# Performance work log

Measured on AMD Instinct MI355X. Metric: run time of the kernel, lower is better.

Reference implementation:

```python
import jax, jax.numpy as jnp
import numpy as np

VOCAB, X, H, C_CLS = 32000, 300, 512, 5
B, N_LEAVES = 256, 256  # complete binary trees, depth 9, 511 nodes/tree

def setup_inputs() -> dict:
    key = jax.random.key(0)
    ks = jax.random.split(key, 10)
    s = lambda k, shp, fan: jax.random.normal(k, shp, jnp.float32) * (1.0 / np.sqrt(fan))
    return {
        'wordid': jax.random.randint(ks[0], (B, N_LEAVES), 0, VOCAB),
        'emb': jax.random.normal(ks[1], (VOCAB, X), jnp.float32) * 0.1,
        'W_iou_w': s(ks[2], (3 * H, X), X),
        'W_iou_b': jnp.zeros((3 * H,), jnp.float32),
        'U_iou_w': s(ks[3], (3 * H, 2 * H), 2 * H),
        'U_iou_b': jnp.zeros((3 * H,), jnp.float32),
        'U_f_w': s(ks[4], (2 * H, 2 * H), 2 * H),
        'U_f_b': jnp.zeros((2 * H,), jnp.float32),
        'lin_w': s(ks[5], (C_CLS, H), H),
        'lin_b': jnp.zeros((C_CLS,), jnp.float32),
    }

def _cell(iou, c_f):
    i, o, u = jnp.split(iou, 3, axis=-1)
    c = jax.nn.sigmoid(i) * jnp.tanh(u) + c_f
    h = jax.nn.sigmoid(o) * jnp.tanh(c)
    return h, c

def reference(wordid, emb, W_iou_w, W_iou_b, U_iou_w, U_iou_b, U_f_w, U_f_b, lin_w, lin_b):
    b, n = wordid.shape
    # leaves: is_leaf=1 -> iou = W_iou(x), c_f = 0
    x = emb[wordid]                                   # [B, L, X]
    iou = x @ W_iou_w.T + W_iou_b                     # [B, L, 3H]
    h, c = _cell(iou, 0.0)
    hs = [h]
    # internal levels: reduce over exactly 2 children (binary TreeLSTM)
    while h.shape[1] > 1:
        m = h.shape[1] // 2
        h_cat = h.reshape(b, m, 2 * H)                # concat of 2 children
        c_pair = c.reshape(b, m, 2, H)
        f = jax.nn.sigmoid(h_cat @ U_f_w.T + U_f_b).reshape(b, m, 2, H)
        c_f = jnp.sum(f * c_pair, axis=2)             # [B, m, H]
        iou = h_cat @ U_iou_w.T + U_iou_b             # is_leaf=0 branch
        h, c = _cell(iou, c_f)
        hs.append(h)
    h_all = jnp.concatenate(hs, axis=1)               # [B, 2L-1, H], leaves-first topo order
    # dropout is identity at inference
    logits = h_all @ lin_w.T + lin_b                  # [B, 2L-1, num_classes]
    return logits
```

## Files before the change

kernel.cpp:

```cpp
#include <hip/hip_runtime.h>
#include <hip/hip_bf16.h>


typedef __bf16 bf16;
typedef bf16  bf16x8 __attribute__((ext_vector_type(8)));
typedef float f32x4  __attribute__((ext_vector_type(4)));

__device__ __forceinline__ float sigm(float x){ return 1.0f/(1.0f + __expf(-x)); }
__device__ __forceinline__ float tanh_f(float x){ return 1.0f - 2.0f/(__expf(2.0f*x)+1.0f); }

__device__ __forceinline__ void gload16(const bf16* g, bf16* l){
  __builtin_amdgcn_global_load_lds(
      (const __attribute__((address_space(1))) void*)g,
      (__attribute__((address_space(3))) void*)l, 16, 0, 0);
}

#define FENCE_LGKM do{ asm volatile("s_waitcnt lgkmcnt(0)" ::: "memory"); \
  __builtin_amdgcn_sched_barrier(0); __builtin_amdgcn_s_barrier(); \
  __builtin_amdgcn_sched_barrier(0); }while(0)
#define FENCE_VM(N) do{ asm volatile("s_waitcnt vmcnt(" #N ")" ::: "memory"); \
  __builtin_amdgcn_sched_barrier(0); __builtin_amdgcn_s_barrier(); \
  __builtin_amdgcn_sched_barrier(0); }while(0)

__global__ void cvt_all(const float* __restrict__ Wiou, const float* __restrict__ Uiou,
                        const float* __restrict__ Uf, const float* __restrict__ emb,
                        bf16* __restrict__ Wpad, bf16* __restrict__ Uall,
                        bf16* __restrict__ embp){
  const int b = blockIdx.x, t = threadIdx.x;
  if (b < 1536){
    Wpad[b*320 + t] = (bf16)(t < 300 ? Wiou[b*300 + t] : 0.f);
  } else if (b < 1536 + 32000){
    const int r = b - 1536;
    embp[(size_t)r*320 + t] = (bf16)(t < 300 ? emb[(size_t)r*300 + t] : 0.f);
  } else {
    const size_t i = (size_t)(b - 33536)*320 + t;
    if (i < (size_t)1536*1024) Uall[i] = (bf16)Uiou[i];
    else                       Uall[i] = (bf16)Uf[i - (size_t)1536*1024];
  }
}

__global__ __launch_bounds__(256, 2)
void leaf128_kernel(const int* __restrict__ wordid, const bf16* __restrict__ embp,
                    const bf16* __restrict__ Wpad, const float* __restrict__ Wb,
                    bf16* __restrict__ hcur, float* __restrict__ ccur)
{
  __shared__ bf16 lsA[2][128*32];
  __shared__ bf16 lsB[2][192*32];
  const int t = threadIdx.x;
  const int mrow0 = blockIdx.x*128, nblk = blockIdx.y*64;
  const int lane16 = t&15, quad = (t&63)>>4, w = t>>6;

  const int lrow = t>>2;
  const int qsw  = ((t&3) ^ ((t>>3)&3))*8;
  const int wb   = (t & 192)*8;

  const int wid0 = wordid[mrow0 + lrow];
  const int wid1 = wordid[mrow0 + 64 + lrow];
  const bf16* srcA0 = embp + (size_t)wid0*320 + qsw;
  const bf16* srcA1 = embp + (size_t)wid1*320 + qsw;
  const bf16* srcB0 = Wpad + (size_t)(0*512 + nblk + lrow)*320 + qsw;
  const bf16* srcB1 = Wpad + (size_t)(1*512 + nblk + lrow)*320 + qsw;
  const bf16* srcB2 = Wpad + (size_t)(2*512 + nblk + lrow)*320 + qsw;

  const int sA   = (t>>1)&3;
  const int aoff = lane16*32 + ((quad ^ sA)*8);
  const int boff = (w*16 + lane16)*32 + ((quad ^ sA)*8);

  f32x4 acc[3][8];
  const f32x4 zero = {0.f,0.f,0.f,0.f};
  #pragma unroll
  for(int o=0;o<3;o++){
    #pragma unroll
    for(int rt=0;rt<8;rt++) acc[o][rt]=zero;
  }

  {
    gload16(srcA0     , lsA[0] + wb);        gload16(srcA1     , lsA[0] + 2048 + wb);
    gload16(srcB0     , lsB[0] + wb);        gload16(srcB1     , lsB[0] + 2048 + wb);
    gload16(srcB2     , lsB[0] + 4096 + wb);
    gload16(srcA0 + 32, lsA[1] + wb);        gload16(srcA1 + 32, lsA[1] + 2048 + wb);
    gload16(srcB0 + 32, lsB[1] + wb);        gload16(srcB1 + 32, lsB[1] + 2048 + wb);
    gload16(srcB2 + 32, lsB[1] + 4096 + wb);
  }
  FENCE_VM(5);

  for (int ks = 0; ks < 10; ks++){
    const int cur = ks & 1;
    bf16x8 bfrag[3], afrag[8];
    #pragma unroll
    for(int g=0;g<3;g++) bfrag[g] = *(const bf16x8*)&lsB[cur][g*2048 + boff];
    #pragma unroll
    for(int rt=0;rt<8;rt++) afrag[rt] = *(const bf16x8*)&lsA[cur][rt*512 + aoff];
    FENCE_LGKM;
    if (ks < 8){
      const int k0 = (ks+2)*32;
      gload16(srcA0 + k0, lsA[cur] + wb);        gload16(srcA1 + k0, lsA[cur] + 2048 + wb);
      gload16(srcB0 + k0, lsB[cur] + wb);        gload16(srcB1 + k0, lsB[cur] + 2048 + wb);
      gload16(srcB2 + k0, lsB[cur] + 4096 + wb);
    }
    __builtin_amdgcn_s_setprio(1);
    #pragma unroll
    for(int rt=0;rt<8;rt++){
      #pragma unroll
      for(int g=0;g<3;g++)
        acc[g][rt] = __builtin_amdgcn_mfma_f32_16x16x32_bf16(afrag[rt], bfrag[g], acc[g][rt], 0,0,0);
    }
    __builtin_amdgcn_s_setprio(0);
    if (ks < 8)      FENCE_VM(5);
    else if (ks < 9) FENCE_VM(0);
  }
  const int j = nblk + w*16 + lane16;
  const float bi=Wb[j], bo=Wb[512+j], bu=Wb[1024+j];
  #pragma unroll
  for(int rt=0;rt<8;rt++){
    #pragma unroll
    for(int reg=0;reg<4;reg++){
      const int row = mrow0 + rt*16 + quad*4 + reg;
      float iv=acc[0][rt][reg]+bi, ov=acc[1][rt][reg]+bo, uv=acc[2][rt][reg]+bu;
      float c = sigm(iv)*tanh_f(uv);
      float h = sigm(ov)*tanh_f(c);
      ccur[(size_t)row*512 + j] = c;
      hcur[(size_t)row*512 + j] = (bf16)h;
    }
  }
}

__global__ __launch_bounds__(256)
void level_kernel(const bf16* __restrict__ hprev, bf16* __restrict__ hcur,
                  const float* __restrict__ cprev, float* __restrict__ ccur,
                  const bf16* __restrict__ Uall, const float* __restrict__ Uioub,
                  const float* __restrict__ Ufb)
{
  __shared__ bf16 lsA[64*40];
  __shared__ bf16 lsB[5][64*40];
  const int t = threadIdx.x;
  const int mrow0 = blockIdx.x*64, nblk = blockIdx.y*64;
  const int r = t>>2, kc = (t&3)*8;
  const int lane16 = t&15, quad = (t&63)>>4, w = t>>6;

  f32x4 acc[5][4];
  const f32x4 zero = {0.f,0.f,0.f,0.f};
  #pragma unroll
  for(int o=0;o<5;o++){
    #pragma unroll
    for(int rt=0;rt<4;rt++) acc[o][rt]=zero;
  }

  const bf16* arow = hprev + (size_t)(mrow0 + r)*1024;
  const int col = nblk + r;
  for (int k0=0;k0<1024;k0+=32){
    *(bf16x8*)&lsA[r*40+kc] = *(const bf16x8*)&arow[k0+kc];
    #pragma unroll
    for(int g=0;g<5;g++)
      *(bf16x8*)&lsB[g][r*40+kc] = *(const bf16x8*)&Uall[(size_t)(g*512+col)*1024 + k0+kc];
    __syncthreads();
    bf16x8 bfrag[5];
    #pragma unroll
    for(int o=0;o<5;o++) bfrag[o] = *(const bf16x8*)&lsB[o][(w*16+lane16)*40 + quad*8];
    #pragma unroll
    for(int rt=0;rt<4;rt++){
      bf16x8 a = *(const bf16x8*)&lsA[(rt*16+lane16)*40 + quad*8];
      #pragma unroll
      for(int o=0;o<5;o++)
        acc[o][rt] = __builtin_amdgcn_mfma_f32_16x16x32_bf16(a, bfrag[o], acc[o][rt], 0,0,0);
    }
    __syncthreads();
  }
  const int j = nblk + w*16 + lane16;
  const float bi =Uioub[j], bo=Uioub[512+j], bu=Uioub[1024+j];
  const float bfl=Ufb[j],   bfr=Ufb[512+j];
  #pragma unroll
  for(int rt=0;rt<4;rt++){
    #pragma unroll
    for(int reg=0;reg<4;reg++){
      const int row = mrow0 + rt*16 + quad*4 + reg;
      float iv=acc[0][rt][reg]+bi, ov=acc[1][rt][reg]+bo, uv=acc[2][rt][reg]+bu;
      float fl=acc[3][rt][reg]+bfl, fr=acc[4][rt][reg]+bfr;
      float cl = cprev[((size_t)row*2  )*512 + j];
      float cr = cprev[((size_t)row*2+1)*512 + j];
      float cf = sigm(fl)*cl + sigm(fr)*cr;
      float c  = sigm(iv)*tanh_f(uv) + cf;
      float h  = sigm(ov)*tanh_f(c);
      ccur[(size_t)row*512 + j] = c;
      hcur[(size_t)row*512 + j] = (bf16)h;
    }
  }
}

__global__ __launch_bounds__(256, 2)
void level128_kernel(const bf16* __restrict__ hprev, bf16* __restrict__ hcur,
                     const float* __restrict__ cprev, float* __restrict__ ccur,
                     const bf16* __restrict__ Uall, const float* __restrict__ Uioub,
                     const float* __restrict__ Ufb)
{
  __shared__ bf16 lsA[2][128*32];
  __shared__ bf16 lsB[2][320*32];
  const int t = threadIdx.x;
  const int mrow0 = blockIdx.x*128, nblk = blockIdx.y*64;
  const int lane16 = t&15, quad = (t&63)>>4, w = t>>6;

  const int lrow = t>>2;
  const int qsw  = ((t&3) ^ ((t>>3)&3))*8;
  const int wb   = (t & 192)*8;

  const bf16* srcA0 = hprev + (size_t)(mrow0 + lrow)*1024 + qsw;
  const bf16* srcA1 = hprev + (size_t)(mrow0 + 64 + lrow)*1024 + qsw;
  const bf16* srcB0 = Uall + (size_t)(0*512 + nblk + lrow)*1024 + qsw;
  const bf16* srcB1 = Uall + (size_t)(1*512 + nblk + lrow)*1024 + qsw;
  const bf16* srcB2 = Uall + (size_t)(2*512 + nblk + lrow)*1024 + qsw;
  const bf16* srcB3 = Uall + (size_t)(3*512 + nblk + lrow)*1024 + qsw;
  const bf16* srcB4 = Uall + (size_t)(4*512 + nblk + lrow)*1024 + qsw;

  const int sA   = (t>>1)&3;
  const int aoff = lane16*32 + ((quad ^ sA)*8);
  const int boff = (w*16 + lane16)*32 + ((quad ^ sA)*8);

  f32x4 acc[5][8];
  const f32x4 zero = {0.f,0.f,0.f,0.f};
  #pragma unroll
  for(int o=0;o<5;o++){
    #pragma unroll
    for(int rt=0;rt<8;rt++) acc[o][rt]=zero;
  }

  {
    gload16(srcA0     , lsA[0] + wb);        gload16(srcA1     , lsA[0] + 2048 + wb);
    gload16(srcB0     , lsB[0] + wb);        gload16(srcB1     , lsB[0] + 2048 + wb);
    gload16(srcB2     , lsB[0] + 4096 + wb); gload16(srcB3     , lsB[0] + 6144 + wb);
    gload16(srcB4     , lsB[0] + 8192 + wb);
    gload16(srcA0 + 32, lsA[1] + wb);        gload16(srcA1 + 32, lsA[1] + 2048 + wb);
    gload16(srcB0 + 32, lsB[1] + wb);        gload16(srcB1 + 32, lsB[1] + 2048 + wb);
    gload16(srcB2 + 32, lsB[1] + 4096 + wb); gload16(srcB3 + 32, lsB[1] + 6144 + wb);
    gload16(srcB4 + 32, lsB[1] + 8192 + wb);
  }
  FENCE_VM(7);

  for (int ks = 0; ks < 32; ks++){
    const int cur = ks & 1;
    bf16x8 bfrag[5], afrag[8];
    #pragma unroll
    for(int g=0;g<5;g++) bfrag[g] = *(const bf16x8*)&lsB[cur][g*2048 + boff];
    #pragma unroll
    for(int rt=0;rt<8;rt++) afrag[rt] = *(const bf16x8*)&lsA[cur][rt*512 + aoff];
    FENCE_LGKM;
    if (ks < 30){
      const int k0 = (ks+2)*32;
      gload16(srcA0 + k0, lsA[cur] + wb);        gload16(srcA1 + k0, lsA[cur] + 2048 + wb);
      gload16(srcB0 + k0, lsB[cur] + wb);        gload16(srcB1 + k0, lsB[cur] + 2048 + wb);
      gload16(srcB2 + k0, lsB[cur] + 4096 + wb); gload16(srcB3 + k0, lsB[cur] + 6144 + wb);
      gload16(srcB4 + k0, lsB[cur] + 8192 + wb);
    }
    __builtin_amdgcn_s_setprio(1);
    #pragma unroll
    for(int rt=0;rt<8;rt++){
      #pragma unroll
      for(int g=0;g<5;g++)
        acc[g][rt] = __builtin_amdgcn_mfma_f32_16x16x32_bf16(afrag[rt], bfrag[g], acc[g][rt], 0,0,0);
    }
    __builtin_amdgcn_s_setprio(0);
    if (ks < 30)      FENCE_VM(7);
    else if (ks < 31) FENCE_VM(0);
  }
  const int j = nblk + w*16 + lane16;
  const float bi =Uioub[j], bo=Uioub[512+j], bu=Uioub[1024+j];
  const float bfl=Ufb[j],   bfr=Ufb[512+j];
  #pragma unroll
  for(int rt=0;rt<8;rt++){
    #pragma unroll
    for(int reg=0;reg<4;reg++){
      const int row = mrow0 + rt*16 + quad*4 + reg;
      float iv=acc[0][rt][reg]+bi, ov=acc[1][rt][reg]+bo, uv=acc[2][rt][reg]+bu;
      float fl=acc[3][rt][reg]+bfl, fr=acc[4][rt][reg]+bfr;
      float cl = cprev[((size_t)row*2  )*512 + j];
      float cr = cprev[((size_t)row*2+1)*512 + j];
      float cf = sigm(fl)*cl + sigm(fr)*cr;
      float c  = sigm(iv)*tanh_f(uv) + cf;
      float h  = sigm(ov)*tanh_f(c);
      ccur[(size_t)row*512 + j] = c;
      hcur[(size_t)row*512 + j] = (bf16)h;
    }
  }
}

__global__ __launch_bounds__(256)
void logits_kernel(const bf16* __restrict__ h, const float* __restrict__ linw,
                   const float* __restrict__ linb, float* __restrict__ out,
                   int rowbase, int lgm, int mask, int off){
  const int row = blockIdx.x*4 + (threadIdx.x>>6);
  const int l = threadIdx.x & 63;
  bf16x8 hv = *(const bf16x8*)(h + (size_t)row*512 + l*8);
  float hf[8];
  #pragma unroll
  for(int jj=0;jj<8;jj++) hf[jj] = (float)hv[jj];
  float s[5];
  #pragma unroll
  for(int c=0;c<5;c++){
    const f32x4 w0 = *(const f32x4*)(linw + c*512 + l*8);
    const f32x4 w1 = *(const f32x4*)(linw + c*512 + l*8 + 4);
    float a = 0.f;
    #pragma unroll
    for(int jj=0;jj<4;jj++) a += hf[jj]*w0[jj] + hf[4+jj]*w1[jj];
    s[c]=a;
  }
  #pragma unroll
  for(int o=32;o>0;o>>=1){
    #pragma unroll
    for(int c=0;c<5;c++) s[c] += __shfl_down(s[c], o, 64);
  }
  if (l==0){
    const int g = rowbase + row;
    const int node = (g>>lgm)*511 + off + (g&mask);
    #pragma unroll
    for(int c=0;c<5;c++) out[(size_t)node*5+c] = s[c] + linb[c];
  }
}

__global__ __launch_bounds__(256)
void logits2_kernel(const bf16* __restrict__ ha, int rows_a, int lgm_a, int mask_a, int off_a,
                    const bf16* __restrict__ hb, int lgm_b, int mask_b, int off_b,
                    const float* __restrict__ linw, const float* __restrict__ linb,
                    float* __restrict__ out){
  const int row = blockIdx.x*4 + (threadIdx.x>>6);
  const int l = threadIdx.x & 63;
  const bf16* hrow; int g, lgm, mask, off;
  if (row < rows_a){ hrow = ha + (size_t)row*512;            g = row;           lgm=lgm_a; mask=mask_a; off=off_a; }
  else             { hrow = hb + (size_t)(row-rows_a)*512;   g = row - rows_a;  lgm=lgm_b; mask=mask_b; off=off_b; }
  bf16x8 hv = *(const bf16x8*)(hrow + l*8);
  float hf[8];
  #pragma unroll
  for(int jj=0;jj<8;jj++) hf[jj] = (float)hv[jj];
  float s[5];
  #pragma unroll
  for(int c=0;c<5;c++){
    const f32x4 w0 = *(const f32x4*)(linw + c*512 + l*8);
    const f32x4 w1 = *(const f32x4*)(linw + c*512 + l*8 + 4);
    float a = 0.f;
    #pragma unroll
    for(int jj=0;jj<4;jj++) a += hf[jj]*w0[jj] + hf[4+jj]*w1[jj];
    s[c]=a;
  }
  #pragma unroll
  for(int o=32;o>0;o>>=1){
    #pragma unroll
    for(int c=0;c<5;c++) s[c] += __shfl_down(s[c], o, 64);
  }
  if (l==0){
    const int node = (g>>lgm)*511 + off + (g&mask);
    #pragma unroll
    for(int c=0;c<5;c++) out[(size_t)node*5+c] = s[c] + linb[c];
  }
}

__global__ void zero_out(float* out, int n){
  int i = blockIdx.x*256 + threadIdx.x;
  if (i < n) out[i] = 0.f;
}

extern "C" void kernel_launch(void* const* d_in, const int* in_sizes, int n_in,
                              void* d_out, int out_size, void* d_ws, size_t ws_size,
                              hipStream_t stream)
{
  const int*   wordid = (const int*)d_in[0];
  const float* emb    = (const float*)d_in[1];
  const float* Wiou   = (const float*)d_in[2];
  const float* Wioub  = (const float*)d_in[3];
  const float* Uiou   = (const float*)d_in[4];
  const float* Uioub  = (const float*)d_in[5];
  const float* Uf     = (const float*)d_in[6];
  const float* Ufb    = (const float*)d_in[7];
  const float* linw   = (const float*)d_in[8];
  const float* linb   = (const float*)d_in[9];
  float* out = (float*)d_out;

  const size_t oWPD  = 0;
  const size_t oUALL = oWPD  + (size_t)1536*320*2;
  const size_t oEMB  = oUALL + (size_t)2560*1024*2;
  const size_t oH1   = oEMB  + (size_t)32000*320*2;
  const size_t oC1   = oH1   + (size_t)32768*512*2;
  const size_t oH0   = oC1   + (size_t)32768*512*4;
  size_t R0 = 0;
  {
    const size_t t2 = oH0 + (size_t)32768*512*(2+4);
    const size_t t4 = oH0 + (size_t)16384*512*(2+4);
    const size_t t8 = oH0 + (size_t) 8192*512*(2+4);
    if      (ws_size >= t2) R0 = 32768;
    else if (ws_size >= t4) R0 = 16384;
    else if (ws_size >= t8) R0 = 8192;
  }
  if (R0 == 0){
    zero_out<<<(out_size+255)/256, 256, 0, stream>>>(out, out_size);
    return;
  }

  char* ws = (char*)d_ws;
  bf16*  Wpad = (bf16*)(ws + oWPD);
  bf16*  Uall = (bf16*)(ws + oUALL);
  bf16*  embp = (bf16*)(ws + oEMB);
  bf16*  h1   = (bf16*)(ws + oH1);
  float* c1   = (float*)(ws + oC1);
  bf16*  h0   = (bf16*)(ws + oH0);
  float* c0   = (float*)(ws + oH0 + R0*1024);

  cvt_all<<<41728, 320, 0, stream>>>(Wiou, Uiou, Uf, emb, Wpad, Uall, embp);

  const int offs[9] = {0,256,384,448,480,496,504,508,510};
  const int nchunk = (int)(65536 / R0);

  for (int ch = 0; ch < nchunk; ch++){
    const int* wid = wordid + (size_t)ch*R0;
    leaf128_kernel<<<dim3((int)(R0/128), 8), 256, 0, stream>>>(wid, embp, Wpad, Wioub,
                                                               h0, c0);
    logits_kernel<<<(int)(R0/4), 256, 0, stream>>>(h0, linw, linb, out,
                                                   (int)(ch*R0), 8, 255, 0);
    bf16*  h1c = h1 + (size_t)ch*(R0/2)*512;
    float* c1c = c1 + (size_t)ch*(R0/2)*512;
    const int orows = (int)(R0/2);
    level128_kernel<<<dim3(orows/128, 8), 256, 0, stream>>>(h0, h1c, c0, c1c,
                                                            Uall, Uioub, Ufb);
  }

  for (int lv = 2; lv <= 8; lv++){
    const int rows = 65536 >> lv;
    const bf16*  hin  = (lv & 1) ? h0 : h1;
    bf16*        hout = (lv & 1) ? h1 : h0;
    const float* cin  = (lv & 1) ? c0 : c1;
    float*       cout = (lv & 1) ? c1 : c0;
    if (rows >= 8192)
      level128_kernel<<<dim3(rows/128, 8), 256, 0, stream>>>(hin, hout, cin, cout,
                                                             Uall, Uioub, Ufb);
    else
      level_kernel<<<dim3(rows/64, 8), 256, 0, stream>>>(hin, hout, cin, cout,
                                                         Uall, Uioub, Ufb);
    if ((lv & 1) == 0){
      const int rows_a = 65536 >> (lv-1);
      const int rows_b = rows;
      logits2_kernel<<<(rows_a + rows_b)/4, 256, 0, stream>>>(
          h1, rows_a, 8-(lv-1), (256>>(lv-1))-1, offs[lv-1],
          h0,         8-lv,     (256>>lv)-1,     offs[lv],
          linw, linb, out);
    }
  }
}
```

Before: 846.3 us.

## Double-buffer MFMA fragments in registers and restructure LDS/DMA pipeline

Rewrites the K-loops of the leaf and level128 GEMM kernels into a manually unrolled ping-pong schedule. Fragments for the next K-slice are read from LDS into a second register set while MFMAs run on the current set, and the next global-to-LDS DMA is issued in the same window. Barriers are now tied to vmcnt waits rather than separate lgkm fences. The level128 launch bound is relaxed from 2 to 1 blocks per SM to leave room for the extra fragment registers, which risks lower occupancy. The DMA now effectively prefetches only one stage ahead, since it waits on vmcnt(0) each half-step.

```diff
diff --git a/kernel.cpp b/kernel.cpp
--- a/kernel.cpp
+++ b/kernel.cpp
@@ -15,12 +15,12 @@
       (__attribute__((address_space(3))) void*)l, 16, 0, 0);
 }
 
-#define FENCE_LGKM do{ asm volatile("s_waitcnt lgkmcnt(0)" ::: "memory"); \
+#define VMBAR(N) do{ asm volatile("s_waitcnt vmcnt(" #N ")" ::: "memory"); \
   __builtin_amdgcn_sched_barrier(0); __builtin_amdgcn_s_barrier(); \
   __builtin_amdgcn_sched_barrier(0); }while(0)
-#define FENCE_VM(N) do{ asm volatile("s_waitcnt vmcnt(" #N ")" ::: "memory"); \
-  __builtin_amdgcn_sched_barrier(0); __builtin_amdgcn_s_barrier(); \
+#define LGKM0 do{ asm volatile("s_waitcnt lgkmcnt(0)" ::: "memory"); \
   __builtin_amdgcn_sched_barrier(0); }while(0)
+#define SBAR0 __builtin_amdgcn_sched_barrier(0)
 
 __global__ void cvt_all(const float* __restrict__ Wiou, const float* __restrict__ Uiou,
                         const float* __restrict__ Uf, const float* __restrict__ emb,
@@ -66,6 +66,18 @@
   const int aoff = lane16*32 + ((quad ^ sA)*8);
   const int boff = (w*16 + lane16)*32 + ((quad ^ sA)*8);
 
+#define LEAF_DMA(buf, k0) do{ \
+  gload16(srcA0 + (k0), lsA[buf] + wb);        gload16(srcA1 + (k0), lsA[buf] + 2048 + wb); \
+  gload16(srcB0 + (k0), lsB[buf] + wb);        gload16(srcB1 + (k0), lsB[buf] + 2048 + wb); \
+  gload16(srcB2 + (k0), lsB[buf] + 4096 + wb); }while(0)
+#define LEAF_READ(buf, A, Bv) do{ \
+  _Pragma("unroll") for(int g=0;g<3;g++) Bv[g] = *(const bf16x8*)&lsB[buf][g*2048 + boff]; \
+  _Pragma("unroll") for(int rt=0;rt<8;rt++) A[rt] = *(const bf16x8*)&lsA[buf][rt*512 + aoff]; }while(0)
+#define LEAF_MFMA(A, Bv) do{ __builtin_amdgcn_s_setprio(1); \
+  _Pragma("unroll") for(int rt=0;rt<8;rt++){ _Pragma("unroll") for(int g=0;g<3;g++) \
+    acc[g][rt] = __builtin_amdgcn_mfma_f32_16x16x32_bf16(A[rt], Bv[g], acc[g][rt], 0,0,0); } \
+  __builtin_amdgcn_s_setprio(0); }while(0)
+
   f32x4 acc[3][8];
   const f32x4 zero = {0.f,0.f,0.f,0.f};
   #pragma unroll
@@ -73,42 +85,34 @@
     #pragma unroll
     for(int rt=0;rt<8;rt++) acc[o][rt]=zero;
   }
-
-  {
-    gload16(srcA0     , lsA[0] + wb);        gload16(srcA1     , lsA[0] + 2048 + wb);
-    gload16(srcB0     , lsB[0] + wb);        gload16(srcB1     , lsB[0] + 2048 + wb);
-    gload16(srcB2     , lsB[0] + 4096 + wb);
-    gload16(srcA0 + 32, lsA[1] + wb);        gload16(srcA1 + 32, lsA[1] + 2048 + wb);
-    gload16(srcB0 + 32, lsB[1] + wb);        gload16(srcB1 + 32, lsB[1] + 2048 + wb);
-    gload16(srcB2 + 32, lsB[1] + 4096 + wb);
-  }
-  FENCE_VM(5);
-
-  for (int ks = 0; ks < 10; ks++){
-    const int cur = ks & 1;
-    bf16x8 bfrag[3], afrag[8];
-    #pragma unroll
-    for(int g=0;g<3;g++) bfrag[g] = *(const bf16x8*)&lsB[cur][g*2048 + boff];
-    #pragma unroll
-    for(int rt=0;rt<8;rt++) afrag[rt] = *(const bf16x8*)&lsA[cur][rt*512 + aoff];
-    FENCE_LGKM;
-    if (ks < 8){
-      const int k0 = (ks+2)*32;
-      gload16(srcA0 + k0, lsA[cur] + wb);        gload16(srcA1 + k0, lsA[cur] + 2048 + wb);
-      gload16(srcB0 + k0, lsB[cur] + wb);        gload16(srcB1 + k0, lsB[cur] + 2048 + wb);
-      gload16(srcB2 + k0, lsB[cur] + 4096 + wb);
-    }
-    __builtin_amdgcn_s_setprio(1);
-    #pragma unroll
-    for(int rt=0;rt<8;rt++){
-      #pragma unroll
-      for(int g=0;g<3;g++)
-        acc[g][rt] = __builtin_amdgcn_mfma_f32_16x16x32_bf16(afrag[rt], bfrag[g], acc[g][rt], 0,0,0);
-    }
-    __builtin_amdgcn_s_setprio(0);
-    if (ks < 8)      FENCE_VM(5);
-    else if (ks < 9) FENCE_VM(0);
-  }
+  bf16x8 fA[8], fB[3], gA[8], gB[3];
+
+  LEAF_DMA(0, 0); LEAF_DMA(1, 32);
+  VMBAR(5);
+  LEAF_READ(0, fA, fB);
+  LGKM0;
+
+  for (int kk = 0; kk < 8; kk += 2){
+    VMBAR(0);
+    LEAF_DMA(0, (kk+2)*32);
+    LEAF_READ(1, gA, gB);
+    SBAR0;
+    LEAF_MFMA(fA, fB);
+    LGKM0;
+    VMBAR(0);
+    LEAF_DMA(1, (kk+3)*32);
+    LEAF_READ(0, fA, fB);
+    SBAR0;
+    LEAF_MFMA(gA, gB);
+    LGKM0;
+  }
+  VMBAR(0);
+  LEAF_READ(1, gA, gB);
+  SBAR0;
+  LEAF_MFMA(fA, fB);
+  LGKM0;
+  LEAF_MFMA(gA, gB);
+
   const int j = nblk + w*16 + lane16;
   const float bi=Wb[j], bo=Wb[512+j], bu=Wb[1024+j];
   #pragma unroll
@@ -123,6 +127,9 @@
       hcur[(size_t)row*512 + j] = (bf16)h;
     }
   }
+#undef LEAF_DMA
+#undef LEAF_READ
+#undef LEAF_MFMA
 }
 
 __global__ __launch_bounds__(256)
@@ -187,7 +194,7 @@
   }
 }
 
-__global__ __launch_bounds__(256, 2)
+__global__ __launch_bounds__(256, 1)
 void level128_kernel(const bf16* __restrict__ hprev, bf16* __restrict__ hcur,
                      const float* __restrict__ cprev, float* __restrict__ ccur,
                      const bf16* __restrict__ Uall, const float* __restrict__ Uioub,
@@ -215,6 +222,19 @@
   const int aoff = lane16*32 + ((quad ^ sA)*8);
   const int boff = (w*16 + lane16)*32 + ((quad ^ sA)*8);
 
+#define LVL_DMA(buf, k0) do{ \
+  gload16(srcA0 + (k0), lsA[buf] + wb);        gload16(srcA1 + (k0), lsA[buf] + 2048 + wb); \
+  gload16(srcB0 + (k0), lsB[buf] + wb);        gload16(srcB1 + (k0), lsB[buf] + 2048 + wb); \
+  gload16(srcB2 + (k0), lsB[buf] + 4096 + wb); gload16(srcB3 + (k0), lsB[buf] + 6144 + wb); \
+  gload16(srcB4 + (k0), lsB[buf] + 8192 + wb); }while(0)
+#define LVL_READ(buf, A, Bv) do{ \
+  _Pragma("unroll") for(int g=0;g<5;g++) Bv[g] = *(const bf16x8*)&lsB[buf][g*2048 + boff]; \
+  _Pragma("unroll") for(int rt=0;rt<8;rt++) A[rt] = *(const bf16x8*)&lsA[buf][rt*512 + aoff]; }while(0)
+#define LVL_MFMA(A, Bv) do{ __builtin_amdgcn_s_setprio(1); \
+  _Pragma("unroll") for(int rt=0;rt<8;rt++){ _Pragma("unroll") for(int g=0;g<5;g++) \
+    acc[g][rt] = __builtin_amdgcn_mfma_f32_16x16x32_bf16(A[rt], Bv[g], acc[g][rt], 0,0,0); } \
+  __builtin_amdgcn_s_setprio(0); }while(0)
+
   f32x4 acc[5][8];
   const f32x4 zero = {0.f,0.f,0.f,0.f};
   #pragma unroll
@@ -222,45 +242,34 @@
     #pragma unroll
     for(int rt=0;rt<8;rt++) acc[o][rt]=zero;
   }
-
-  {
-    gload16(srcA0     , lsA[0] + wb);        gload16(srcA1     , lsA[0] + 2048 + wb);
-    gload16(srcB0     , lsB[0] + wb);        gload16(srcB1     , lsB[0] + 2048 + wb);
-    gload16(srcB2     , lsB[0] + 4096 + wb); gload16(srcB3     , lsB[0] + 6144 + wb);
-    gload16(srcB4     , lsB[0] + 8192 + wb);
-    gload16(srcA0 + 32, lsA[1] + wb);        gload16(srcA1 + 32, lsA[1] + 2048 + wb);
-    gload16(srcB0 + 32, lsB[1] + wb);        gload16(srcB1 + 32, lsB[1] + 2048 + wb);
-    gload16(srcB2 + 32, lsB[1] + 4096 + wb); gload16(srcB3 + 32, lsB[1] + 6144 + wb);
-    gload16(srcB4 + 32, lsB[1] + 8192 + wb);
-  }
-  FENCE_VM(7);
-
-  for (int ks = 0; ks < 32; ks++){
-    const int cur = ks & 1;
-    bf16x8 bfrag[5], afrag[8];
-    #pragma unroll
-    for(int g=0;g<5;g++) bfrag[g] = *(const bf16x8*)&lsB[cur][g*2048 + boff];
-    #pragma unroll
-    for(int rt=0;rt<8;rt++) afrag[rt] = *(const bf16x8*)&lsA[cur][rt*512 + aoff];
-    FENCE_LGKM;
-    if (ks < 30){
-      const int k0 = (ks+2)*32;
-      gload16(srcA0 + k0, lsA[cur] + wb);        gload16(srcA1 + k0, lsA[cur] + 2048 + wb);
-      gload16(srcB0 + k0, lsB[cur] + wb);        gload16(srcB1 + k0, lsB[cur] + 2048 + wb);
-      gload16(srcB2 + k0, lsB[cur] + 4096 + wb); gload16(srcB3 + k0, lsB[cur] + 6144 + wb);
-      gload16(srcB4 + k0, lsB[cur] + 8192 + wb);
-    }
-    __builtin_amdgcn_s_setprio(1);
-    #pragma unroll
-    for(int rt=0;rt<8;rt++){
-      #pragma unroll
-      for(int g=0;g<5;g++)
-        acc[g][rt] = __builtin_amdgcn_mfma_f32_16x16x32_bf16(afrag[rt], bfrag[g], acc[g][rt], 0,0,0);
-    }
-    __builtin_amdgcn_s_setprio(0);
-    if (ks < 30)      FENCE_VM(7);
-    else if (ks < 31) FENCE_VM(0);
-  }
+  bf16x8 fA[8], fB[5], gA[8], gB[5];
+
+  LVL_DMA(0, 0); LVL_DMA(1, 32);
+  VMBAR(7);
+  LVL_READ(0, fA, fB);
+  LGKM0;
+
+  for (int kk = 0; kk < 30; kk += 2){
+    VMBAR(0);
+    LVL_DMA(0, (kk+2)*32);
+    LVL_READ(1, gA, gB);
+    SBAR0;
+    LVL_MFMA(fA, fB);
+    LGKM0;
+    VMBAR(0);
+    LVL_DMA(1, (kk+3)*32);
+    LVL_READ(0, fA, fB);
+    SBAR0;
+    LVL_MFMA(gA, gB);
+    LGKM0;
+  }
+  VMBAR(0);
+  LVL_READ(1, gA, gB);
+  SBAR0;
+  LVL_MFMA(fA, fB);
+  LGKM0;
+  LVL_MFMA(gA, gB);
+
   const int j = nblk + w*16 + lane16;
   const float bi =Uioub[j], bo=Uioub[512+j], bu=Uioub[1024+j];
   const float bfl=Ufb[j],   bfr=Ufb[512+j];
@@ -280,6 +289,9 @@
       hcur[(size_t)row*512 + j] = (bf16)h;
     }
   }
+#undef LVL_DMA
+#undef LVL_READ
+#undef LVL_MFMA
 }
 
 __global__ __launch_bounds__(256)
```

New measurement: 1.028 ms. 21.5% more time.
